# Optimization experiments

Hardware: AMD Instinct MI355X
Metric: run time of the kernel (lower is better)

The kernel has to match this reference:

```python
import jax, jax.numpy as jnp
import numpy as np
import math

DIM = 256; SEQ = 2048; BSZ = 32; NI = 128; NS = 4; ITERS = 3

def _ln(x, g, b):
    m = x.mean(-1, keepdims=True)
    v = ((x - m) ** 2).mean(-1, keepdims=True)
    return (x - m) / jnp.sqrt(v + 1e-5) * g + b

def _norm(x):
    # torch F.normalize: x / ||x||.clamp_min(1e-12)
    return x / jnp.clip(jnp.linalg.norm(x, axis=-1, keepdims=True), 1e-12, None)

def setup_inputs() -> dict:
    key = jax.random.key(0)
    ks = jax.random.split(key, 16)
    def w(k, shape, s=0.02):
        return jax.random.normal(k, shape, jnp.float32) * s
    return {
        'tokens': jax.random.normal(ks[0], (BSZ, SEQ, DIM), jnp.float32),
        'cls_embed': jax.random.normal(ks[1], (BSZ, DIM), jnp.float32),
        'intent_queries': jax.random.normal(ks[2], (NI, DIM), jnp.float32),
        'noise': jax.random.normal(ks[3], (NI, BSZ, NS, DIM), jnp.float32),
        'Wk': w(ks[4], (DIM, DIM)), 'bk': jnp.zeros(DIM, jnp.float32),
        'Wv': w(ks[5], (DIM, DIM)), 'bv': jnp.zeros(DIM, jnp.float32),
        'Wqs': w(ks[6], (DIM, DIM)), 'bqs': jnp.zeros(DIM, jnp.float32),
        'Wqi': w(ks[7], (DIM, DIM)), 'bqi': jnp.zeros(DIM, jnp.float32),
        'ln1_g': jnp.ones(DIM, jnp.float32), 'ln1_b': jnp.zeros(DIM, jnp.float32),
        'ln2_g': jnp.ones(DIM, jnp.float32), 'ln2_b': jnp.zeros(DIM, jnp.float32),
        'Wf1': w(ks[8], (DIM, 2 * DIM)), 'bf1': jnp.zeros(2 * DIM, jnp.float32),
        'Wf2': w(ks[9], (2 * DIM, DIM)), 'bf2': jnp.zeros(DIM, jnp.float32),
        'slot_mu': w(ks[10], (1, NS, DIM)),  # randn*0.02
        'slot_sigma': jnp.ones((1, NS, DIM), jnp.float32) * 0.1,
        'alpha': jnp.float32(1.0),
        'temperature': jnp.float32(1.0),
    }

def reference(tokens, cls_embed, intent_queries, noise, Wk, bk, Wv, bv,
              Wqs, bqs, Wqi, bqi, ln1_g, ln1_b, ln2_g, ln2_b,
              Wf1, bf1, Wf2, bf2, slot_mu, slot_sigma, alpha, temperature):
    scale = 1.0 / math.sqrt(DIM)
    # k/v are identical across the per-intent loop in the original -> compute once
    k = tokens @ Wk + bk  # [B,S,D]
    v = tokens @ Wv + bv  # [B,S,D]
    cls_n = _norm(cls_embed)  # [B,D]

    def per_intent(q, eps):  # q: [D], eps: [B,NS,D]
        qn = _norm(q)
        q_intent = (q @ Wqi + bqi)[None, None, :]  # broadcast over [B,NS,:]
        slots = slot_mu[0] + eps * slot_sigma[0]   # [B,NS,D]
        for _ in range(ITERS):
            q_slot = slots @ Wqs + bqs + q_intent
            logit = jnp.einsum('bnd,bsd->bns', q_slot, k) * scale
            attn = jax.nn.softmax(logit, axis=-1)
            upd = jnp.einsum('bns,bsd->bnd', attn, v)
            slots = _ln(slots + upd, ln1_g, ln1_b)
            h = _ln(slots, ln2_g, ln2_b)
            slots = slots + jax.nn.gelu(h @ Wf1 + bf1, approximate=False) @ Wf2 + bf2
        sn = _norm(slots)                               # [B,NS,D]
        a = jax.nn.softmax(jnp.einsum('bnd,d->bn', sn, qn), axis=-1)
        summ = jnp.einsum('bn,bnd->bd', a, slots)       # slot_summary
        fused = cls_n + alpha * _norm(summ)
        return fused @ qn                               # [B]

    scores = jax.vmap(per_intent)(intent_queries, noise)  # [NI,B]
    logits = scores.T / jnp.maximum(temperature, 1e-4)    # [B,NI]
    return logits
```

## Files before the change

kernel.cpp:

```cpp
#include <hip/hip_runtime.h>
#include <math.h>

#define BSZ 32
#define NI  128

typedef __attribute__((ext_vector_type(8))) _Float16 f16x8;
typedef __attribute__((ext_vector_type(4))) _Float16 f16x4;
typedef __attribute__((ext_vector_type(4))) float    f32x4;

#define MFMA16(a, b, c) __builtin_amdgcn_mfma_f32_16x16x32_f16((a), (b), (c), 0, 0, 0)

#define GLL(g, l) __builtin_amdgcn_global_load_lds(                          \
    (const __attribute__((address_space(1))) void*)(g),                      \
    (__attribute__((address_space(3))) void*)(l), 16, 0, 0)

#define LGKM_BAR() do {                                                      \
    asm volatile("s_waitcnt lgkmcnt(0)" ::: "memory");                       \
    __builtin_amdgcn_sched_barrier(0);                                       \
    __builtin_amdgcn_s_barrier();                                            \
    __builtin_amdgcn_sched_barrier(0); } while (0)

__device__ inline float dot4f(float4 a, float4 b) {
    return a.x * b.x + a.y * b.y + a.z * b.z + a.w * b.w;
}

__device__ inline float4* slp(float* base, int r, int c) {
    return (float4*)(base + r * 256 + ((((c) >> 2) ^ (r & 7)) << 2));
}

__device__ inline void tpose64(const float* __restrict__ src, int Csrc,
                               _Float16* __restrict__ dstT, int KT,
                               int r0, int c0, _Float16 (*tbuf)[72], int tid)
{
#pragma unroll
    for (int it = 0; it < 4; it++) {
        int idx = tid + it * 256;
        int rr = idx >> 4, c4 = idx & 15;
        float4 w = *(const float4*)(src + (size_t)(r0 + rr) * Csrc + c0 + c4 * 4);
        tbuf[c4 * 4 + 0][rr] = (_Float16)w.x;
        tbuf[c4 * 4 + 1][rr] = (_Float16)w.y;
        tbuf[c4 * 4 + 2][rr] = (_Float16)w.z;
        tbuf[c4 * 4 + 3][rr] = (_Float16)w.w;
    }
    __syncthreads();
#pragma unroll
    for (int it = 0; it < 2; it++) {
        int idx = tid + it * 256;
        int orr = idx >> 3, oc8 = idx & 7;
        int n = c0 + orr;
        size_t tile = (size_t)(n >> 4) * KT + (r0 >> 5) + (oc8 >> 2);
        *(f16x8*)(dstT + tile * 512 + (n & 15) * 32 + (oc8 & 3) * 8) = *(const f16x8*)&tbuf[orr][oc8 * 8];
    }
}

__global__ __launch_bounds__(256) void prep(
    const float* __restrict__ Wk, const float* __restrict__ Wv,
    const float* __restrict__ Wqs, const float* __restrict__ Wf1,
    const float* __restrict__ Wf2,
    const float* __restrict__ intent_q, const float* __restrict__ Wqi,
    const float* __restrict__ bqi, const float* __restrict__ bqs,
    const float* __restrict__ cls_embed,
    _Float16* __restrict__ wkT, _Float16* __restrict__ wvT,
    _Float16* __restrict__ wqsT, _Float16* __restrict__ wf1T,
    _Float16* __restrict__ wf2T,
    float* __restrict__ qint2, float* __restrict__ qn, float* __restrict__ clsn)
{
    __shared__ _Float16 tbuf[64][72];
    __shared__ float buf[256];
    __shared__ float red[4];
    const int t = threadIdx.x, blk = blockIdx.x;
    const int lane = t & 63, w = t >> 6;

    if (blk < 112) {
        if (blk < 16)       tpose64(Wk, 256, wkT, 8, (blk >> 2) * 64, (blk & 3) * 64, tbuf, t);
        else if (blk < 32)  { int tt = blk - 16; tpose64(Wv, 256, wvT, 8, (tt >> 2) * 64, (tt & 3) * 64, tbuf, t); }
        else if (blk < 48)  { int tt = blk - 32; tpose64(Wqs, 256, wqsT, 8, (tt >> 2) * 64, (tt & 3) * 64, tbuf, t); }
        else if (blk < 80)  { int tt = blk - 48; tpose64(Wf1, 512, wf1T, 8, (tt & 3) * 64, (tt >> 2) * 64, tbuf, t); }
        else                { int tt = blk - 80; tpose64(Wf2, 256, wf2T, 16, (tt >> 2) * 64, (tt & 3) * 64, tbuf, t); }
    } else if (blk < 240) {
        int i = blk - 112;
        float x = intent_q[(size_t)i * 256 + t];
        buf[t] = x;
        float ss = x * x;
#pragma unroll
        for (int m = 1; m < 64; m <<= 1) ss += __shfl_xor(ss, m, 64);
        if (lane == 0) red[w] = ss;
        __syncthreads();
        float tot = red[0] + red[1] + red[2] + red[3];
        qn[(size_t)i * 256 + t] = x / fmaxf(sqrtf(tot), 1e-12f);
        float acc = bqi[t] + bqs[t];
        for (int e = 0; e < 256; e += 4) {
            const float4 q4 = *(const float4*)&buf[e];
            acc += q4.x * Wqi[(size_t)(e + 0) * 256 + t];
            acc += q4.y * Wqi[(size_t)(e + 1) * 256 + t];
            acc += q4.z * Wqi[(size_t)(e + 2) * 256 + t];
            acc += q4.w * Wqi[(size_t)(e + 3) * 256 + t];
        }
        qint2[(size_t)i * 256 + t] = acc;
    } else {
        int b = blk - 240;
        float x = cls_embed[(size_t)b * 256 + t];
        float ss = x * x;
#pragma unroll
        for (int m = 1; m < 64; m <<= 1) ss += __shfl_xor(ss, m, 64);
        if (lane == 0) red[w] = ss;
        __syncthreads();
        float tot = red[0] + red[1] + red[2] + red[3];
        clsn[(size_t)b * 256 + t] = x / fmaxf(sqrtf(tot), 1e-12f);
    }
}

__global__ __launch_bounds__(512, 2) void kvf_k(
    const float* __restrict__ tokens,
    const _Float16* __restrict__ wkT, const _Float16* __restrict__ wvT,
    const float* __restrict__ bk, const float* __restrict__ bv,
    _Float16* __restrict__ kT, _Float16* __restrict__ vT)
{
    __shared__ __align__(16) _Float16 Sb[2][8192];

    const int t = threadIdx.x, lane = t & 63, w = t >> 6;
    const int l15 = lane & 15, quad = lane >> 4;
    const int lofs = l15 * 32 + quad * 8;
    const int lofsA = ((l15 * 4 + quad) ^ ((l15 >> 1) & 7)) * 8;
    const int bx = blockIdx.x;
    const int b = bx & 31, chunk = bx >> 5;

    f16x8 wk[2][8], wv[2][8];
#pragma unroll
    for (int j = 0; j < 2; j++)
#pragma unroll
        for (int ks = 0; ks < 8; ks++) {
            wk[j][ks] = *(const f16x8*)(wkT + ((size_t)(2 * w + j) * 8 + ks) * 512 + lofs);
            wv[j][ks] = *(const f16x8*)(wvT + ((size_t)(2 * w + j) * 8 + ks) * 512 + lofs);
        }
    f32x4 bi0 = *(const f32x4*)(bk + w * 32 + quad * 4);
    f32x4 bi1 = *(const f32x4*)(bk + w * 32 + 16 + quad * 4);
    const float bv0 = bv[(2 * w) * 16 + l15];
    const float bv1 = bv[(2 * w + 1) * 16 + l15];

    const int rr = t >> 5, d8 = t & 31;
    const float* tbase = tokens + ((size_t)b * 2048 + chunk * 256) * 256 + rr * 256 + d8 * 8;
    const int mskW = ((rr >> 1) & 7) ^ (((d8 >> 2) & 3) << 1);
    const int wofs0 = (d8 >> 2) * 512 + (((rr * 4 + (d8 & 3)) ^ mskW) * 8);
    const int wofs1 = wofs0 + 8 * 512;

    float4 pa0, pa1, pb0, pb1;

#define KVF_LOADS(P) do {                                                    \
        const float* sp_ = tbase + (size_t)(P) * 8192;                       \
        pa0 = *(const float4*)(sp_);                                         \
        pa1 = *(const float4*)(sp_ + 4);                                     \
        pb0 = *(const float4*)(sp_ + 4096);                                  \
        pb1 = *(const float4*)(sp_ + 4100);                                  \
    } while (0)

#define KVF_STAGE(BUF) do {                                                  \
        f16x8 h0, h1;                                                        \
        h0[0] = (_Float16)pa0.x; h0[1] = (_Float16)pa0.y;                    \
        h0[2] = (_Float16)pa0.z; h0[3] = (_Float16)pa0.w;                    \
        h0[4] = (_Float16)pa1.x; h0[5] = (_Float16)pa1.y;                    \
        h0[6] = (_Float16)pa1.z; h0[7] = (_Float16)pa1.w;                    \
        h1[0] = (_Float16)pb0.x; h1[1] = (_Float16)pb0.y;                    \
        h1[2] = (_Float16)pb0.z; h1[3] = (_Float16)pb0.w;                    \
        h1[4] = (_Float16)pb1.x; h1[5] = (_Float16)pb1.y;                    \
        h1[6] = (_Float16)pb1.z; h1[7] = (_Float16)pb1.w;                    \
        *(f16x8*)((BUF) + wofs0) = h0;                                       \
        *(f16x8*)((BUF) + wofs1) = h1;                                       \
    } while (0)

    KVF_LOADS(0);
    KVF_STAGE(&Sb[0][0]);
    LGKM_BAR();

    for (int p = 0; p < 8; p++) {
        if (p < 7) KVF_LOADS(p + 1);
        __builtin_amdgcn_sched_barrier(0);

        const _Float16* lb = &Sb[p & 1][0];
        const int stg0 = chunk * 16 + p * 2;
        const int sp = chunk * 8 + p;

        f16x8 a[2][8];
#pragma unroll
        for (int st = 0; st < 2; st++)
#pragma unroll
            for (int ks = 0; ks < 8; ks++)
                a[st][ks] = *(const f16x8*)(lb + (st * 8 + ks) * 512 + (lofsA ^ ((ks & 3) * 16)));

#pragma unroll
        for (int st = 0; st < 2; st++) {
            f32x4 c0 = {0.f, 0.f, 0.f, 0.f}, c1 = {0.f, 0.f, 0.f, 0.f};
#pragma unroll
            for (int ks = 0; ks < 8; ks++) {
                c0 = MFMA16(wk[0][ks], a[st][ks], c0);
                c1 = MFMA16(wk[1][ks], a[st][ks], c1);
            }
            f16x4 p0, p1;
#pragma unroll
            for (int reg = 0; reg < 4; reg++) {
                p0[reg] = (_Float16)(c0[reg] + bi0[reg]);
                p1[reg] = (_Float16)(c1[reg] + bi1[reg]);
            }
            _Float16* tp = kT + ((size_t)(b * 128 + stg0 + st) * 8 + w) * 512 + l15 * 32;
            *(f16x4*)(tp + (quad >> 1) * 8 + (quad & 1) * 4) = p0;
            *(f16x4*)(tp + (2 + (quad >> 1)) * 8 + (quad & 1) * 4) = p1;
        }

#pragma unroll
        for (int j = 0; j < 2; j++) {
            f32x4 c0 = {0.f, 0.f, 0.f, 0.f}, c1 = {0.f, 0.f, 0.f, 0.f};
#pragma unroll
            for (int ks = 0; ks < 8; ks++) {
                c0 = MFMA16(a[0][ks], wv[j][ks], c0);
                c1 = MFMA16(a[1][ks], wv[j][ks], c1);
            }
            const float bb = j ? bv1 : bv0;
            f16x4 p0, p1;
#pragma unroll
            for (int reg = 0; reg < 4; reg++) {
                p0[reg] = (_Float16)(c0[reg] + bb);
                p1[reg] = (_Float16)(c1[reg] + bb);
            }
            _Float16* tp = vT + ((size_t)(b * 16 + 2 * w + j) * 64 + sp) * 512 + l15 * 32;
            *(f16x4*)(tp + (quad >> 1) * 8 + (quad & 1) * 4) = p0;
            *(f16x4*)(tp + (2 + (quad >> 1)) * 8 + (quad & 1) * 4) = p1;
        }

        if (p < 7) {
            KVF_STAGE(&Sb[(p + 1) & 1][0]);
            LGKM_BAR();
        }
    }
#undef KVF_LOADS
#undef KVF_STAGE
}

__global__ __launch_bounds__(256, 4) void slotq_k(
    const float* __restrict__ noise, const float* __restrict__ slot_mu,
    const float* __restrict__ slot_sigma,
    const _Float16* __restrict__ wqsT, const float* __restrict__ qint2,
    float* __restrict__ slots, _Float16* __restrict__ qsT)
{
    __shared__ float sb[16 * 256];
    const int tid = threadIdx.x, lane = tid & 63, w4 = tid >> 6;
    const int l15 = lane & 15, quad = lane >> 4;
    const int lofs = l15 * 32 + quad * 8;
    const int rt = blockIdx.x;
    const int gr0 = rt * 16;

    {
        const int lr = w4 * 4 + quad;
        const int gr = gr0 + lr;
        const int b = gr >> 9, i = (gr >> 2) & 127, n = gr & 3;
        const float* np = noise + (((size_t)i * BSZ + b) * 4 + n) * 256;
#pragma unroll
        for (int k = 0; k < 4; k++) {
            const int c = k * 64 + l15 * 4;
            float4 mu = *(const float4*)(slot_mu + n * 256 + c);
            float4 sg = *(const float4*)(slot_sigma + n * 256 + c);
            float4 ns = *(const float4*)(np + c);
            float4 o;
            o.x = mu.x + ns.x * sg.x; o.y = mu.y + ns.y * sg.y;
            o.z = mu.z + ns.z * sg.z; o.w = mu.w + ns.w * sg.w;
            *slp(sb, lr, c) = o;
            *(float4*)(slots + (size_t)gr * 256 + c) = o;
        }
    }
    __syncthreads();

    f16x8 bs[8];
#pragma unroll
    for (int ks = 0; ks < 8; ks++) {
        const int c0 = ks * 32 + quad * 8;
        float4 xa = *slp(sb, l15, c0);
        float4 xb = *slp(sb, l15, c0 + 4);
        bs[ks][0] = (_Float16)xa.x; bs[ks][1] = (_Float16)xa.y;
        bs[ks][2] = (_Float16)xa.z; bs[ks][3] = (_Float16)xa.w;
        bs[ks][4] = (_Float16)xb.x; bs[ks][5] = (_Float16)xb.y;
        bs[ks][6] = (_Float16)xb.z; bs[ks][7] = (_Float16)xb.w;
    }
    const int iq = ((gr0 + l15) & 511) >> 2;
#pragma unroll
    for (int d = 0; d < 4; d++) {
        const int dti = w4 * 4 + d;
        f32x4 c = {0.f, 0.f, 0.f, 0.f};
#pragma unroll
        for (int ks = 0; ks < 8; ks++)
            c = MFMA16(*(const f16x8*)(wqsT + ((size_t)dti * 8 + ks) * 512 + lofs), bs[ks], c);
        float4 qi = *(const float4*)(qint2 + (size_t)iq * 256 + dti * 16 + quad * 4);
        f16x4 o;
#pragma unroll
        for (int reg = 0; reg < 4; reg++) o[reg] = (_Float16)((c[reg] + qi[reg]) * 0.0625f);
        *(f16x4*)(qsT + ((size_t)rt * 8 + (dti >> 1)) * 512 + l15 * 32
                  + ((dti & 1) * 2 + (quad >> 1)) * 8 + (quad & 1) * 4) = o;
    }
}

__global__ __launch_bounds__(512, 4) void attn_k(
    const _Float16* __restrict__ qsT, const _Float16* __restrict__ kT,
    const _Float16* __restrict__ vT,
    _Float16* __restrict__ Opart, float* __restrict__ psum4)
{
    __shared__ __align__(16) _Float16 arena[24576];
    __shared__ __align__(16) _Float16 pb[8][640];

    _Float16* KbA = arena;
    _Float16* VbA = arena + 16384;

    const int tid = threadIdx.x, lane = tid & 63, wv = tid >> 6;
    const int l15 = lane & 15, quad = lane >> 4;
    const int lofs = l15 * 32 + quad * 8;
    const int lofsA = ((l15 * 4 + quad) ^ ((l15 >> 1) & 7)) * 8;
    const int lnsw = (lane ^ ((lane >> 3) & 7)) * 8;
    const int bx = blockIdx.x;
    const int b = bx & 31, rb = (bx >> 5) & 3, sk = bx >> 7;
    const int gr0 = b * 512 + rb * 128 + wv * 16;
    const int rt_q = gr0 >> 4;

    _Float16* pw = pb[wv];

    const _Float16* kSrc = kT + ((size_t)(b * 128 + sk * 32) * 8) * 512;
    const _Float16* vSrc = vT + ((size_t)(b * 16) * 64 + sk * 16) * 512;

#pragma unroll
    for (int j = 0; j < 2; j++) {
        const int ee = wv * 2 + j;
        GLL(kSrc + (size_t)((ee >> 3) * 8 + (ee & 7)) * 512 + lnsw,
            KbA + ee * 512 + lane * 8);
    }

    f16x8 q[8];
#pragma unroll
    for (int ks = 0; ks < 8; ks++)
        q[ks] = *(const f16x8*)(qsT + ((size_t)rt_q * 8 + ks) * 512 + lofs);

    f32x4 O[16];
#pragma unroll
    for (int dt = 0; dt < 16; dt++) O[dt] = (f32x4){0.f, 0.f, 0.f, 0.f};
    float ps[4] = {0.f, 0.f, 0.f, 0.f};

    asm volatile("s_waitcnt vmcnt(0)" ::: "memory");
    __builtin_amdgcn_s_barrier();
    __builtin_amdgcn_sched_barrier(0);

    for (int ss = 0; ss < 16; ss++) {
        const int cur = ss & 1;

#pragma unroll
        for (int j = 0; j < 2; j++) {
            const int ee = wv * 2 + j;
            GLL(vSrc + (size_t)(ee * 64 + ss) * 512 + lnsw, VbA + ee * 512 + lane * 8);
        }
        if (ss < 15) {
#pragma unroll
            for (int j = 0; j < 2; j++) {
                const int ee = wv * 2 + j;
                GLL(kSrc + (size_t)((2 * (ss + 1) + (ee >> 3)) * 8 + (ee & 7)) * 512 + lnsw,
                    KbA + (cur ^ 1) * 8192 + ee * 512 + lane * 8);
            }
            asm volatile("s_waitcnt vmcnt(4)" ::: "memory");
        } else {
            asm volatile("s_waitcnt vmcnt(2)" ::: "memory");
        }
        __builtin_amdgcn_s_barrier();
        __builtin_amdgcn_sched_barrier(0);

#pragma unroll
        for (int kt = 0; kt < 2; kt++) {
            const _Float16* kp = KbA + cur * 8192 + (kt * 8) * 512;
            f32x4 c0 = {0.f, 0.f, 0.f, 0.f};
#pragma unroll
            for (int ks = 0; ks < 8; ks++)
                c0 = MFMA16(q[ks], *(const f16x8*)(kp + ks * 512 + lofsA), c0);
            const int col = kt * 16 + l15;
#pragma unroll
            for (int reg = 0; reg < 4; reg++) {
                float p0 = __expf(fminf(c0[reg], 10.5f));
                ps[reg] += p0;
                pw[(quad * 4 + reg) * 40 + col] = (_Float16)p0;
            }
        }

        __builtin_amdgcn_sched_barrier(0);
        asm volatile("s_waitcnt lgkmcnt(0)" ::: "memory");
        if (ss < 15) {
            asm volatile("s_waitcnt vmcnt(2)" ::: "memory");
        } else {
            asm volatile("s_waitcnt vmcnt(0)" ::: "memory");
        }
        __builtin_amdgcn_s_barrier();
        __builtin_amdgcn_sched_barrier(0);

        {
            f16x8 pa = *(const f16x8*)(pw + l15 * 40 + quad * 8);
#pragma unroll
            for (int dt = 0; dt < 16; dt++)
                O[dt] = MFMA16(pa, *(const f16x8*)(VbA + dt * 512 + lofsA), O[dt]);
        }
        __builtin_amdgcn_sched_barrier(0);
        __builtin_amdgcn_s_barrier();
        __builtin_amdgcn_sched_barrier(0);
    }

#pragma unroll
    for (int msk = 1; msk <= 8; msk <<= 1)
#pragma unroll
        for (int reg = 0; reg < 4; reg++) ps[reg] += __shfl_xor(ps[reg], msk, 64);
    if (l15 == 0) {
#pragma unroll
        for (int reg = 0; reg < 4; reg++)
            psum4[(size_t)sk * 16384 + gr0 + quad * 4 + reg] = ps[reg];
    }

    _Float16* ow = arena + wv * 2176;
#pragma unroll
    for (int hd = 0; hd < 2; hd++) {
#pragma unroll
        for (int dt = 0; dt < 8; dt++) {
            const int dti = hd * 8 + dt;
#pragma unroll
            for (int reg = 0; reg < 4; reg++)
                ow[(quad * 4 + reg) * 136 + dt * 16 + l15] = (_Float16)O[dti][reg];
        }
#pragma unroll
        for (int p2 = 0; p2 < 4; p2++) {
            const int u = lane + p2 * 64;
            const int row = u >> 4, col8 = u & 15;
            *(f16x8*)(Opart + ((size_t)sk * 16384 + gr0 + row) * 256 + hd * 128 + col8 * 8) =
                *(const f16x8*)(ow + row * 136 + col8 * 8);
        }
    }
}

__global__ __launch_bounds__(256, 4) void mlp_k(
    const _Float16* __restrict__ Opart, const float* __restrict__ psum4,
    float* __restrict__ slots,
    const float* __restrict__ ln1_g, const float* __restrict__ ln1_b,
    const float* __restrict__ ln2_g, const float* __restrict__ ln2_b,
    const _Float16* __restrict__ wf1T, const float* __restrict__ bf1,
    const _Float16* __restrict__ wf2T, const float* __restrict__ bf2,
    const _Float16* __restrict__ wqsT, const float* __restrict__ qint2,
    _Float16* __restrict__ qsT,
    const float* __restrict__ qn, const float* __restrict__ clsn,
    const float* __restrict__ alphap, const float* __restrict__ tempp,
    float* __restrict__ out, int it)
{
    __shared__ float sl[16 * 256];
    __shared__ float2 st2[16];
    __shared__ __align__(16) _Float16 actL[8192];

    const int tid = threadIdx.x, lane = tid & 63, w4 = tid >> 6;
    const int l15 = lane & 15, quad = lane >> 4;
    const int lofs = l15 * 32 + quad * 8;
    const int lofsA = ((l15 * 4 + quad) ^ ((l15 >> 1) & 7)) * 8;
    const int bx = blockIdx.x;
    const int b = bx & 31, rg = bx >> 5;
    const int R0 = b * 512 + rg * 16;

    {
        const int lr = w4 * 4 + quad;
        const int gr = R0 + lr;
        float l = 0.f;
#pragma unroll
        for (int j = 0; j < 4; j++) l += psum4[(size_t)j * 16384 + gr];
        const float invl = 1.f / l;
        float4 y[4];
        float sm = 0.f, sq = 0.f;
#pragma unroll
        for (int k = 0; k < 4; k++) {
            const int c = k * 64 + l15 * 4;
            float4 o4 = {0.f, 0.f, 0.f, 0.f};
#pragma unroll
            for (int j = 0; j < 4; j++) {
                f16x4 p = *(const f16x4*)(Opart + ((size_t)j * 16384 + gr) * 256 + c);
                o4.x += (float)p[0]; o4.y += (float)p[1];
                o4.z += (float)p[2]; o4.w += (float)p[3];
            }
            float4 s4 = *(const float4*)(slots + (size_t)gr * 256 + c);
            y[k].x = s4.x + o4.x * invl; y[k].y = s4.y + o4.y * invl;
            y[k].z = s4.z + o4.z * invl; y[k].w = s4.w + o4.w * invl;
            sm += y[k].x + y[k].y + y[k].z + y[k].w;
            sq += dot4f(y[k], y[k]);
        }
#pragma unroll
        for (int m = 1; m <= 8; m <<= 1) { sm += __shfl_xor(sm, m, 64); sq += __shfl_xor(sq, m, 64); }
        const float mean = sm * (1.f / 256.f);
        const float rstd = rsqrtf(sq * (1.f / 256.f) - mean * mean + 1e-5f);
        float sm2 = 0.f, sq2 = 0.f;
#pragma unroll
        for (int k = 0; k < 4; k++) {
            const int c = k * 64 + l15 * 4;
            float4 g1 = *(const float4*)(ln1_g + c);
            float4 b1 = *(const float4*)(ln1_b + c);
            float4 x1;
            x1.x = (y[k].x - mean) * rstd * g1.x + b1.x;
            x1.y = (y[k].y - mean) * rstd * g1.y + b1.y;
            x1.z = (y[k].z - mean) * rstd * g1.z + b1.z;
            x1.w = (y[k].w - mean) * rstd * g1.w + b1.w;
            *slp(sl, lr, c) = x1;
            sm2 += x1.x + x1.y + x1.z + x1.w;
            sq2 += dot4f(x1, x1);
        }
#pragma unroll
        for (int m = 1; m <= 8; m <<= 1) { sm2 += __shfl_xor(sm2, m, 64); sq2 += __shfl_xor(sq2, m, 64); }
        const float mean2 = sm2 * (1.f / 256.f);
        const float rstd2 = rsqrtf(sq2 * (1.f / 256.f) - mean2 * mean2 + 1e-5f);
        if (l15 == 0) st2[lr] = make_float2(mean2, rstd2);
    }
    __syncthreads();

    {
        const float2 s2 = st2[l15];
        f16x8 bh[8];
#pragma unroll
        for (int ks = 0; ks < 8; ks++) {
            const int c0 = ks * 32 + quad * 8;
            float4 xa = *slp(sl, l15, c0);
            float4 xb = *slp(sl, l15, c0 + 4);
            float4 ga = *(const float4*)(ln2_g + c0);
            float4 gb = *(const float4*)(ln2_g + c0 + 4);
            float4 ba = *(const float4*)(ln2_b + c0);
            float4 bb2 = *(const float4*)(ln2_b + c0 + 4);
            bh[ks][0] = (_Float16)((xa.x - s2.x) * s2.y * ga.x + ba.x);
            bh[ks][1] = (_Float16)((xa.y - s2.x) * s2.y * ga.y + ba.y);
            bh[ks][2] = (_Float16)((xa.z - s2.x) * s2.y * ga.z + ba.z);
            bh[ks][3] = (_Float16)((xa.w - s2.x) * s2.y * ga.w + ba.w);
            bh[ks][4] = (_Float16)((xb.x - s2.x) * s2.y * gb.x + bb2.x);
            bh[ks][5] = (_Float16)((xb.y - s2.x) * s2.y * gb.y + bb2.y);
            bh[ks][6] = (_Float16)((xb.z - s2.x) * s2.y * gb.z + bb2.z);
            bh[ks][7] = (_Float16)((xb.w - s2.x) * s2.y * gb.w + bb2.w);
        }
#pragma unroll 2
        for (int t8 = 0; t8 < 8; t8++) {
            const int hti = w4 * 8 + t8;
            f32x4 c = {0.f, 0.f, 0.f, 0.f};
#pragma unroll
            for (int ks = 0; ks < 8; ks++)
                c = MFMA16(*(const f16x8*)(wf1T + ((size_t)hti * 8 + ks) * 512 + lofs), bh[ks], c);
            float4 bb = *(const float4*)(bf1 + hti * 16 + quad * 4);
            f16x4 o;
#pragma unroll
            for (int reg = 0; reg < 4; reg++) {
                float xg = c[reg] + bb[reg];
                o[reg] = (_Float16)(0.5f * xg * (1.f + erff(xg * 0.70710678118654752f)));
            }
            const int gA = l15 * 4 + (hti & 1) * 2 + (quad >> 1);
            *(f16x4*)(actL + ((size_t)(hti >> 1)) * 512
                      + ((gA ^ ((l15 >> 1) & 7)) * 8) + (quad & 1) * 4) = o;
        }
    }
    __syncthreads();

    {
        f32x4 c[4];
#pragma unroll
        for (int d = 0; d < 4; d++) {
            const int dti = w4 * 4 + d;
            float4 x4 = *slp(sl, l15, dti * 16 + quad * 4);
            float4 bb = *(const float4*)(bf2 + dti * 16 + quad * 4);
            c[d] = (f32x4){x4.x + bb.x, x4.y + bb.y, x4.z + bb.z, x4.w + bb.w};
        }
        for (int ks = 0; ks < 16; ks++) {
            f16x8 afrag = *(const f16x8*)(actL + (size_t)ks * 512 + lofsA);
#pragma unroll
            for (int d = 0; d < 4; d++)
                c[d] = MFMA16(*(const f16x8*)(wf2T + ((size_t)(w4 * 4 + d) * 16 + ks) * 512 + lofs),
                              afrag, c[d]);
        }
        __syncthreads();
#pragma unroll
        for (int d = 0; d < 4; d++) {
            const int dti = w4 * 4 + d;
            float4 v = {c[d][0], c[d][1], c[d][2], c[d][3]};
            *slp(sl, l15, dti * 16 + quad * 4) = v;
        }
    }
    __syncthreads();

    if (it < 2) {
        f16x8 bs[8];
#pragma unroll
        for (int ks = 0; ks < 8; ks++) {
            const int c0 = ks * 32 + quad * 8;
            float4 xa = *slp(sl, l15, c0);
            float4 xb = *slp(sl, l15, c0 + 4);
            bs[ks][0] = (_Float16)xa.x; bs[ks][1] = (_Float16)xa.y;
            bs[ks][2] = (_Float16)xa.z; bs[ks][3] = (_Float16)xa.w;
            bs[ks][4] = (_Float16)xb.x; bs[ks][5] = (_Float16)xb.y;
            bs[ks][6] = (_Float16)xb.z; bs[ks][7] = (_Float16)xb.w;
        }
        const int iq = rg * 4 + (l15 >> 2);
        const int rtg = b * 32 + rg;
#pragma unroll
        for (int d = 0; d < 4; d++) {
            const int dti = w4 * 4 + d;
            f32x4 c = {0.f, 0.f, 0.f, 0.f};
#pragma unroll
            for (int ks = 0; ks < 8; ks++)
                c = MFMA16(*(const f16x8*)(wqsT + ((size_t)dti * 8 + ks) * 512 + lofs), bs[ks], c);
            float4 qi = *(const float4*)(qint2 + (size_t)iq * 256 + dti * 16 + quad * 4);
            f16x4 o;
#pragma unroll
            for (int reg = 0; reg < 4; reg++) o[reg] = (_Float16)((c[reg] + qi[reg]) * 0.0625f);
            *(f16x4*)(qsT + ((size_t)rtg * 8 + (dti >> 1)) * 512 + l15 * 32
                      + ((dti & 1) * 2 + (quad >> 1)) * 8 + (quad & 1) * 4) = o;
        }
        {
            const int lr2 = tid >> 4, c16 = tid & 15;
#pragma unroll
            for (int q4 = 0; q4 < 4; q4++) {
                float4 v = *slp(sl, lr2, c16 * 16 + q4 * 4);
                *(float4*)(slots + (size_t)(R0 + lr2) * 256 + c16 * 16 + q4 * 4) = v;
            }
        }
    } else {
        const int i = rg * 4 + w4;
        float4 qv = *(const float4*)(qn + (size_t)i * 256 + lane * 4);
        float4 xs[4];
        float st4[4];
#pragma unroll
        for (int n = 0; n < 4; n++) {
            xs[n] = *slp(sl, w4 * 4 + n, lane * 4);
            float ss = dot4f(xs[n], xs[n]);
            float sq = dot4f(xs[n], qv);
#pragma unroll
            for (int m = 1; m < 64; m <<= 1) { ss += __shfl_xor(ss, m, 64); sq += __shfl_xor(sq, m, 64); }
            st4[n] = sq / fmaxf(sqrtf(ss), 1e-12f);
        }
        float mx = fmaxf(fmaxf(st4[0], st4[1]), fmaxf(st4[2], st4[3]));
        float e0 = __expf(st4[0] - mx), e1 = __expf(st4[1] - mx);
        float e2 = __expf(st4[2] - mx), e3 = __expf(st4[3] - mx);
        float inv = 1.f / (e0 + e1 + e2 + e3);
        float4 smv;
        smv.x = (e0 * xs[0].x + e1 * xs[1].x + e2 * xs[2].x + e3 * xs[3].x) * inv;
        smv.y = (e0 * xs[0].y + e1 * xs[1].y + e2 * xs[2].y + e3 * xs[3].y) * inv;
        smv.z = (e0 * xs[0].z + e1 * xs[1].z + e2 * xs[2].z + e3 * xs[3].z) * inv;
        smv.w = (e0 * xs[0].w + e1 * xs[1].w + e2 * xs[2].w + e3 * xs[3].w) * inv;
        float ssm = dot4f(smv, smv);
        float sqn = dot4f(smv, qv);
        float4 cv = *(const float4*)(clsn + (size_t)b * 256 + lane * 4);
        float cq = dot4f(cv, qv);
#pragma unroll
        for (int m = 1; m < 64; m <<= 1) {
            ssm += __shfl_xor(ssm, m, 64);
            sqn += __shfl_xor(sqn, m, 64);
            cq  += __shfl_xor(cq,  m, 64);
        }
        if (lane == 0) {
            float score = cq + alphap[0] * sqn / fmaxf(sqrtf(ssm), 1e-12f);
            out[(size_t)b * NI + i] = score / fmaxf(tempp[0], 1e-4f);
        }
    }
}

extern "C" void kernel_launch(void* const* d_in, const int* in_sizes, int n_in,
                              void* d_out, int out_size, void* d_ws, size_t ws_size,
                              hipStream_t stream)
{
    const float* tokens     = (const float*)d_in[0];
    const float* cls_embed  = (const float*)d_in[1];
    const float* intent_q   = (const float*)d_in[2];
    const float* noise      = (const float*)d_in[3];
    const float* Wk  = (const float*)d_in[4];
    const float* bk  = (const float*)d_in[5];
    const float* Wv  = (const float*)d_in[6];
    const float* bv  = (const float*)d_in[7];
    const float* Wqs = (const float*)d_in[8];
    const float* bqs = (const float*)d_in[9];
    const float* Wqi = (const float*)d_in[10];
    const float* bqi = (const float*)d_in[11];
    const float* ln1g = (const float*)d_in[12];
    const float* ln1b = (const float*)d_in[13];
    const float* ln2g = (const float*)d_in[14];
    const float* ln2b = (const float*)d_in[15];
    const float* Wf1 = (const float*)d_in[16];
    const float* bf1 = (const float*)d_in[17];
    const float* Wf2 = (const float*)d_in[18];
    const float* bf2 = (const float*)d_in[19];
    const float* slot_mu    = (const float*)d_in[20];
    const float* slot_sigma = (const float*)d_in[21];
    const float* alphap = (const float*)d_in[22];
    const float* tempp  = (const float*)d_in[23];
    float* out = (float*)d_out;

    char* base = (char*)d_ws;
    _Float16* qsT   = (_Float16*)(base);
    _Float16* kT    = (_Float16*)(base + 33554432u);
    _Float16* vT    = (_Float16*)(base + 67108864u);
    _Float16* Opart = (_Float16*)(base + 100663296u);
    float* slots    = (float*)(base + 134217728u);
    _Float16* wkT   = (_Float16*)(base + 150994944u);
    _Float16* wvT   = (_Float16*)(base + 151126016u);
    _Float16* wqsT  = (_Float16*)(base + 151257088u);
    _Float16* wf1T  = (_Float16*)(base + 151388160u);
    _Float16* wf2T  = (_Float16*)(base + 151650304u);
    float* qint2    = (float*)(base + 151912448u);
    float* qnb      = (float*)(base + 152043520u);
    float* clsn     = (float*)(base + 152174592u);
    float* psum4    = (float*)(base + 152207360u);

    prep<<<272, 256, 0, stream>>>(Wk, Wv, Wqs, Wf1, Wf2, intent_q, Wqi, bqi, bqs,
                                  cls_embed, wkT, wvT, wqsT, wf1T, wf2T,
                                  qint2, qnb, clsn);
    kvf_k<<<256, 512, 0, stream>>>(tokens, wkT, wvT, bk, bv, kT, vT);
    slotq_k<<<1024, 256, 0, stream>>>(noise, slot_mu, slot_sigma, wqsT, qint2,
                                      slots, qsT);

    for (int it = 0; it < 3; it++) {
        attn_k<<<512, 512, 0, stream>>>(qsT, kT, vT, Opart, psum4);
        mlp_k<<<1024, 256, 0, stream>>>(Opart, psum4, slots,
                                        ln1g, ln1b, ln2g, ln2b,
                                        wf1T, bf1, wf2T, bf2,
                                        wqsT, qint2, qsT,
                                        qnb, clsn, alphap, tempp, out, it);
    }
}
```

Baseline: 489.3 us.

## Process two 16-row query tiles per wave in attention and MLP kernels

The attention kernel now uses 4 waves per block, each handling 32 query rows (two MFMA row tiles) that share each K and V fragment loaded from LDS. The MLP kernel likewise processes 32 rows per block so each weight fragment fetched from global memory feeds two MFMAs, halving the grid. This cuts LDS and global weight traffic per FLOP but doubles accumulator registers (O[2][16]) and LDS use per block, which may reduce occupancy and parallelism.

```diff
diff --git a/kernel.cpp b/kernel.cpp
--- a/kernel.cpp
+++ b/kernel.cpp
@@ -296,13 +296,13 @@
     }
 }
 
-__global__ __launch_bounds__(512, 4) void attn_k(
+__global__ __launch_bounds__(256, 2) void attn_k(
     const _Float16* __restrict__ qsT, const _Float16* __restrict__ kT,
     const _Float16* __restrict__ vT,
     _Float16* __restrict__ Opart, float* __restrict__ psum4)
 {
     __shared__ __align__(16) _Float16 arena[24576];
-    __shared__ __align__(16) _Float16 pb[8][640];
+    __shared__ __align__(16) _Float16 pb[4][1280];
 
     _Float16* KbA = arena;
     _Float16* VbA = arena + 16384;
@@ -314,7 +314,7 @@
     const int lnsw = (lane ^ ((lane >> 3) & 7)) * 8;
     const int bx = blockIdx.x;
     const int b = bx & 31, rb = (bx >> 5) & 3, sk = bx >> 7;
-    const int gr0 = b * 512 + rb * 128 + wv * 16;
+    const int gr0 = b * 512 + rb * 128 + wv * 32;
     const int rt_q = gr0 >> 4;
 
     _Float16* pw = pb[wv];
@@ -323,21 +323,25 @@
     const _Float16* vSrc = vT + ((size_t)(b * 16) * 64 + sk * 16) * 512;
 
 #pragma unroll
-    for (int j = 0; j < 2; j++) {
-        const int ee = wv * 2 + j;
+    for (int j = 0; j < 4; j++) {
+        const int ee = wv * 4 + j;
         GLL(kSrc + (size_t)((ee >> 3) * 8 + (ee & 7)) * 512 + lnsw,
             KbA + ee * 512 + lane * 8);
     }
 
-    f16x8 q[8];
-#pragma unroll
-    for (int ks = 0; ks < 8; ks++)
-        q[ks] = *(const f16x8*)(qsT + ((size_t)rt_q * 8 + ks) * 512 + lofs);
-
-    f32x4 O[16];
-#pragma unroll
-    for (int dt = 0; dt < 16; dt++) O[dt] = (f32x4){0.f, 0.f, 0.f, 0.f};
-    float ps[4] = {0.f, 0.f, 0.f, 0.f};
+    f16x8 q[2][8];
+#pragma unroll
+    for (int m = 0; m < 2; m++)
+#pragma unroll
+        for (int ks = 0; ks < 8; ks++)
+            q[m][ks] = *(const f16x8*)(qsT + ((size_t)(rt_q + m) * 8 + ks) * 512 + lofs);
+
+    f32x4 O[2][16];
+#pragma unroll
+    for (int m = 0; m < 2; m++)
+#pragma unroll
+        for (int dt = 0; dt < 16; dt++) O[m][dt] = (f32x4){0.f, 0.f, 0.f, 0.f};
+    float ps[2][4] = {{0.f, 0.f, 0.f, 0.f}, {0.f, 0.f, 0.f, 0.f}};
 
     asm volatile("s_waitcnt vmcnt(0)" ::: "memory");
     __builtin_amdgcn_s_barrier();
@@ -347,20 +351,20 @@
         const int cur = ss & 1;
 
 #pragma unroll
-        for (int j = 0; j < 2; j++) {
-            const int ee = wv * 2 + j;
+        for (int j = 0; j < 4; j++) {
+            const int ee = wv * 4 + j;
             GLL(vSrc + (size_t)(ee * 64 + ss) * 512 + lnsw, VbA + ee * 512 + lane * 8);
         }
         if (ss < 15) {
 #pragma unroll
-            for (int j = 0; j < 2; j++) {
-                const int ee = wv * 2 + j;
+            for (int j = 0; j < 4; j++) {
+                const int ee = wv * 4 + j;
                 GLL(kSrc + (size_t)((2 * (ss + 1) + (ee >> 3)) * 8 + (ee & 7)) * 512 + lnsw,
                     KbA + (cur ^ 1) * 8192 + ee * 512 + lane * 8);
             }
+            asm volatile("s_waitcnt vmcnt(8)" ::: "memory");
+        } else {
             asm volatile("s_waitcnt vmcnt(4)" ::: "memory");
-        } else {
-            asm volatile("s_waitcnt vmcnt(2)" ::: "memory");
         }
         __builtin_amdgcn_s_barrier();
         __builtin_amdgcn_sched_barrier(0);
@@ -368,23 +372,29 @@
 #pragma unroll
         for (int kt = 0; kt < 2; kt++) {
             const _Float16* kp = KbA + cur * 8192 + (kt * 8) * 512;
-            f32x4 c0 = {0.f, 0.f, 0.f, 0.f};
-#pragma unroll
-            for (int ks = 0; ks < 8; ks++)
-                c0 = MFMA16(q[ks], *(const f16x8*)(kp + ks * 512 + lofsA), c0);
+            f32x4 c0 = {0.f, 0.f, 0.f, 0.f}, c1 = {0.f, 0.f, 0.f, 0.f};
+#pragma unroll
+            for (int ks = 0; ks < 8; ks++) {
+                f16x8 kf = *(const f16x8*)(kp + ks * 512 + lofsA);
+                c0 = MFMA16(q[0][ks], kf, c0);
+                c1 = MFMA16(q[1][ks], kf, c1);
+            }
             const int col = kt * 16 + l15;
 #pragma unroll
             for (int reg = 0; reg < 4; reg++) {
                 float p0 = __expf(fminf(c0[reg], 10.5f));
-                ps[reg] += p0;
+                float p1 = __expf(fminf(c1[reg], 10.5f));
+                ps[0][reg] += p0;
+                ps[1][reg] += p1;
                 pw[(quad * 4 + reg) * 40 + col] = (_Float16)p0;
+                pw[(16 + quad * 4 + reg) * 40 + col] = (_Float16)p1;
             }
         }
 
         __builtin_amdgcn_sched_barrier(0);
         asm volatile("s_waitcnt lgkmcnt(0)" ::: "memory");
         if (ss < 15) {
-            asm volatile("s_waitcnt vmcnt(2)" ::: "memory");
+            asm volatile("s_waitcnt vmcnt(4)" ::: "memory");
         } else {
             asm volatile("s_waitcnt vmcnt(0)" ::: "memory");
         }
@@ -392,10 +402,14 @@
         __builtin_amdgcn_sched_barrier(0);
 
         {
-            f16x8 pa = *(const f16x8*)(pw + l15 * 40 + quad * 8);
-#pragma unroll
-            for (int dt = 0; dt < 16; dt++)
-                O[dt] = MFMA16(pa, *(const f16x8*)(VbA + dt * 512 + lofsA), O[dt]);
+            f16x8 pa0 = *(const f16x8*)(pw + l15 * 40 + quad * 8);
+            f16x8 pa1 = *(const f16x8*)(pw + (16 + l15) * 40 + quad * 8);
+#pragma unroll
+            for (int dt = 0; dt < 16; dt++) {
+                f16x8 vf = *(const f16x8*)(VbA + dt * 512 + lofsA);
+                O[0][dt] = MFMA16(pa0, vf, O[0][dt]);
+                O[1][dt] = MFMA16(pa1, vf, O[1][dt]);
+            }
         }
         __builtin_amdgcn_sched_barrier(0);
         __builtin_amdgcn_s_barrier();
@@ -403,36 +417,42 @@
     }
 
 #pragma unroll
-    for (int msk = 1; msk <= 8; msk <<= 1)
-#pragma unroll
-        for (int reg = 0; reg < 4; reg++) ps[reg] += __shfl_xor(ps[reg], msk, 64);
-    if (l15 == 0) {
-#pragma unroll
-        for (int reg = 0; reg < 4; reg++)
-            psum4[(size_t)sk * 16384 + gr0 + quad * 4 + reg] = ps[reg];
+    for (int m = 0; m < 2; m++) {
+#pragma unroll
+        for (int msk = 1; msk <= 8; msk <<= 1)
+#pragma unroll
+            for (int reg = 0; reg < 4; reg++) ps[m][reg] += __shfl_xor(ps[m][reg], msk, 64);
+        if (l15 == 0) {
+#pragma unroll
+            for (int reg = 0; reg < 4; reg++)
+                psum4[(size_t)sk * 16384 + gr0 + m * 16 + quad * 4 + reg] = ps[m][reg];
+        }
     }
 
     _Float16* ow = arena + wv * 2176;
 #pragma unroll
-    for (int hd = 0; hd < 2; hd++) {
-#pragma unroll
-        for (int dt = 0; dt < 8; dt++) {
-            const int dti = hd * 8 + dt;
-#pragma unroll
-            for (int reg = 0; reg < 4; reg++)
-                ow[(quad * 4 + reg) * 136 + dt * 16 + l15] = (_Float16)O[dti][reg];
-        }
-#pragma unroll
-        for (int p2 = 0; p2 < 4; p2++) {
-            const int u = lane + p2 * 64;
-            const int row = u >> 4, col8 = u & 15;
-            *(f16x8*)(Opart + ((size_t)sk * 16384 + gr0 + row) * 256 + hd * 128 + col8 * 8) =
-                *(const f16x8*)(ow + row * 136 + col8 * 8);
-        }
-    }
-}
-
-__global__ __launch_bounds__(256, 4) void mlp_k(
+    for (int m = 0; m < 2; m++) {
+#pragma unroll
+        for (int hd = 0; hd < 2; hd++) {
+#pragma unroll
+            for (int dt = 0; dt < 8; dt++) {
+                const int dti = hd * 8 + dt;
+#pragma unroll
+                for (int reg = 0; reg < 4; reg++)
+                    ow[(quad * 4 + reg) * 136 + dt * 16 + l15] = (_Float16)O[m][dti][reg];
+            }
+#pragma unroll
+            for (int p2 = 0; p2 < 4; p2++) {
+                const int u = lane + p2 * 64;
+                const int row = u >> 4, col8 = u & 15;
+                *(f16x8*)(Opart + ((size_t)sk * 16384 + gr0 + m * 16 + row) * 256 + hd * 128 + col8 * 8) =
+                    *(const f16x8*)(ow + row * 136 + col8 * 8);
+            }
+        }
+    }
+}
+
+__global__ __launch_bounds__(256, 2) void mlp_k(
     const _Float16* __restrict__ Opart, const float* __restrict__ psum4,
     float* __restrict__ slots,
     const float* __restrict__ ln1_g, const float* __restrict__ ln1_b,
@@ -445,9 +465,9 @@
     const float* __restrict__ alphap, const float* __restrict__ tempp,
     float* __restrict__ out, int it)
 {
-    __shared__ float sl[16 * 256];
-    __shared__ float2 st2[16];
-    __shared__ __align__(16) _Float16 actL[8192];
+    __shared__ float sl[32 * 256];
+    __shared__ float2 st2[32];
+    __shared__ __align__(16) _Float16 actL[16384];
 
     const int tid = threadIdx.x, lane = tid & 63, w4 = tid >> 6;
     const int l15 = lane & 15, quad = lane >> 4;
@@ -455,10 +475,11 @@
     const int lofsA = ((l15 * 4 + quad) ^ ((l15 >> 1) & 7)) * 8;
     const int bx = blockIdx.x;
     const int b = bx & 31, rg = bx >> 5;
-    const int R0 = b * 512 + rg * 16;
-
-    {
-        const int lr = w4 * 4 + quad;
+    const int R0 = b * 512 + rg * 32;
+
+#pragma unroll
+    for (int r2 = 0; r2 < 2; r2++) {
+        const int lr = w4 * 8 + r2 * 4 + quad;
         const int gr = R0 + lr;
         float l = 0.f;
 #pragma unroll
@@ -510,145 +531,176 @@
     __syncthreads();
 
     {
-        const float2 s2 = st2[l15];
-        f16x8 bh[8];
-#pragma unroll
-        for (int ks = 0; ks < 8; ks++) {
-            const int c0 = ks * 32 + quad * 8;
-            float4 xa = *slp(sl, l15, c0);
-            float4 xb = *slp(sl, l15, c0 + 4);
-            float4 ga = *(const float4*)(ln2_g + c0);
-            float4 gb = *(const float4*)(ln2_g + c0 + 4);
-            float4 ba = *(const float4*)(ln2_b + c0);
-            float4 bb2 = *(const float4*)(ln2_b + c0 + 4);
-            bh[ks][0] = (_Float16)((xa.x - s2.x) * s2.y * ga.x + ba.x);
-            bh[ks][1] = (_Float16)((xa.y - s2.x) * s2.y * ga.y + ba.y);
-            bh[ks][2] = (_Float16)((xa.z - s2.x) * s2.y * ga.z + ba.z);
-            bh[ks][3] = (_Float16)((xa.w - s2.x) * s2.y * ga.w + ba.w);
-            bh[ks][4] = (_Float16)((xb.x - s2.x) * s2.y * gb.x + bb2.x);
-            bh[ks][5] = (_Float16)((xb.y - s2.x) * s2.y * gb.y + bb2.y);
-            bh[ks][6] = (_Float16)((xb.z - s2.x) * s2.y * gb.z + bb2.z);
-            bh[ks][7] = (_Float16)((xb.w - s2.x) * s2.y * gb.w + bb2.w);
+        f16x8 bh[2][8];
+#pragma unroll
+        for (int tt = 0; tt < 2; tt++) {
+            const float2 s2 = st2[tt * 16 + l15];
+#pragma unroll
+            for (int ks = 0; ks < 8; ks++) {
+                const int c0 = ks * 32 + quad * 8;
+                float4 xa = *slp(sl, tt * 16 + l15, c0);
+                float4 xb = *slp(sl, tt * 16 + l15, c0 + 4);
+                float4 ga = *(const float4*)(ln2_g + c0);
+                float4 gb = *(const float4*)(ln2_g + c0 + 4);
+                float4 ba = *(const float4*)(ln2_b + c0);
+                float4 bb2 = *(const float4*)(ln2_b + c0 + 4);
+                bh[tt][ks][0] = (_Float16)((xa.x - s2.x) * s2.y * ga.x + ba.x);
+                bh[tt][ks][1] = (_Float16)((xa.y - s2.x) * s2.y * ga.y + ba.y);
+                bh[tt][ks][2] = (_Float16)((xa.z - s2.x) * s2.y * ga.z + ba.z);
+                bh[tt][ks][3] = (_Float16)((xa.w - s2.x) * s2.y * ga.w + ba.w);
+                bh[tt][ks][4] = (_Float16)((xb.x - s2.x) * s2.y * gb.x + bb2.x);
+                bh[tt][ks][5] = (_Float16)((xb.y - s2.x) * s2.y * gb.y + bb2.y);
+                bh[tt][ks][6] = (_Float16)((xb.z - s2.x) * s2.y * gb.z + bb2.z);
+                bh[tt][ks][7] = (_Float16)((xb.w - s2.x) * s2.y * gb.w + bb2.w);
+            }
         }
 #pragma unroll 2
         for (int t8 = 0; t8 < 8; t8++) {
             const int hti = w4 * 8 + t8;
-            f32x4 c = {0.f, 0.f, 0.f, 0.f};
-#pragma unroll
-            for (int ks = 0; ks < 8; ks++)
-                c = MFMA16(*(const f16x8*)(wf1T + ((size_t)hti * 8 + ks) * 512 + lofs), bh[ks], c);
+            f32x4 c0 = {0.f, 0.f, 0.f, 0.f}, c1 = {0.f, 0.f, 0.f, 0.f};
+#pragma unroll
+            for (int ks = 0; ks < 8; ks++) {
+                f16x8 wfrag = *(const f16x8*)(wf1T + ((size_t)hti * 8 + ks) * 512 + lofs);
+                c0 = MFMA16(wfrag, bh[0][ks], c0);
+                c1 = MFMA16(wfrag, bh[1][ks], c1);
+            }
             float4 bb = *(const float4*)(bf1 + hti * 16 + quad * 4);
-            f16x4 o;
+            f16x4 o0, o1;
 #pragma unroll
             for (int reg = 0; reg < 4; reg++) {
-                float xg = c[reg] + bb[reg];
-                o[reg] = (_Float16)(0.5f * xg * (1.f + erff(xg * 0.70710678118654752f)));
+                float xg0 = c0[reg] + bb[reg];
+                float xg1 = c1[reg] + bb[reg];
+                o0[reg] = (_Float16)(0.5f * xg0 * (1.f + erff(xg0 * 0.70710678118654752f)));
+                o1[reg] = (_Float16)(0.5f * xg1 * (1.f + erff(xg1 * 0.70710678118654752f)));
             }
             const int gA = l15 * 4 + (hti & 1) * 2 + (quad >> 1);
-            *(f16x4*)(actL + ((size_t)(hti >> 1)) * 512
-                      + ((gA ^ ((l15 >> 1) & 7)) * 8) + (quad & 1) * 4) = o;
+            const int aofs = ((size_t)(hti >> 1)) * 512 + ((gA ^ ((l15 >> 1) & 7)) * 8) + (quad & 1) * 4;
+            *(f16x4*)(actL + aofs) = o0;
+            *(f16x4*)(actL + 8192 + aofs) = o1;
         }
     }
     __syncthreads();
 
     {
-        f32x4 c[4];
+        f32x4 c[2][4];
+#pragma unroll
+        for (int tt = 0; tt < 2; tt++)
+#pragma unroll
+            for (int d = 0; d < 4; d++) {
+                const int dti = w4 * 4 + d;
+                float4 x4 = *slp(sl, tt * 16 + l15, dti * 16 + quad * 4);
+                float4 bb = *(const float4*)(bf2 + dti * 16 + quad * 4);
+                c[tt][d] = (f32x4){x4.x + bb.x, x4.y + bb.y, x4.z + bb.z, x4.w + bb.w};
+            }
+        for (int ks = 0; ks < 16; ks++) {
+            f16x8 a0 = *(const f16x8*)(actL + (size_t)ks * 512 + lofsA);
+            f16x8 a1 = *(const f16x8*)(actL + 8192 + (size_t)ks * 512 + lofsA);
+#pragma unroll
+            for (int d = 0; d < 4; d++) {
+                f16x8 wfrag = *(const f16x8*)(wf2T + ((size_t)(w4 * 4 + d) * 16 + ks) * 512 + lofs);
+                c[0][d] = MFMA16(wfrag, a0, c[0][d]);
+                c[1][d] = MFMA16(wfrag, a1, c[1][d]);
+            }
+        }
+        __syncthreads();
+#pragma unroll
+        for (int tt = 0; tt < 2; tt++)
+#pragma unroll
+            for (int d = 0; d < 4; d++) {
+                const int dti = w4 * 4 + d;
+                float4 v = {c[tt][d][0], c[tt][d][1], c[tt][d][2], c[tt][d][3]};
+                *slp(sl, tt * 16 + l15, dti * 16 + quad * 4) = v;
+            }
+    }
+    __syncthreads();
+
+    if (it < 2) {
+        f16x8 bs[2][8];
+#pragma unroll
+        for (int tt = 0; tt < 2; tt++)
+#pragma unroll
+            for (int ks = 0; ks < 8; ks++) {
+                const int c0 = ks * 32 + quad * 8;
+                float4 xa = *slp(sl, tt * 16 + l15, c0);
+                float4 xb = *slp(sl, tt * 16 + l15, c0 + 4);
+                bs[tt][ks][0] = (_Float16)xa.x; bs[tt][ks][1] = (_Float16)xa.y;
+                bs[tt][ks][2] = (_Float16)xa.z; bs[tt][ks][3] = (_Float16)xa.w;
+                bs[tt][ks][4] = (_Float16)xb.x; bs[tt][ks][5] = (_Float16)xb.y;
+                bs[tt][ks][6] = (_Float16)xb.z; bs[tt][ks][7] = (_Float16)xb.w;
+            }
+        const int iq0 = rg * 8 + (l15 >> 2);
+        const int rtg0 = b * 32 + rg * 2;
 #pragma unroll
         for (int d = 0; d < 4; d++) {
             const int dti = w4 * 4 + d;
-            float4 x4 = *slp(sl, l15, dti * 16 + quad * 4);
-            float4 bb = *(const float4*)(bf2 + dti * 16 + quad * 4);
-            c[d] = (f32x4){x4.x + bb.x, x4.y + bb.y, x4.z + bb.z, x4.w + bb.w};
-        }
-        for (int ks = 0; ks < 16; ks++) {
-            f16x8 afrag = *(const f16x8*)(actL + (size_t)ks * 512 + lofsA);
-#pragma unroll
-            for (int d = 0; d < 4; d++)
-                c[d] = MFMA16(*(const f16x8*)(wf2T + ((size_t)(w4 * 4 + d) * 16 + ks) * 512 + lofs),
-                              afrag, c[d]);
-        }
-        __syncthreads();
-#pragma unroll
-        for (int d = 0; d < 4; d++) {
-            const int dti = w4 * 4 + d;
-            float4 v = {c[d][0], c[d][1], c[d][2], c[d][3]};
-            *slp(sl, l15, dti * 16 + quad * 4) = v;
-        }
-    }
-    __syncthreads();
-
-    if (it < 2) {
-        f16x8 bs[8];
-#pragma unroll
-        for (int ks = 0; ks < 8; ks++) {
-            const int c0 = ks * 32 + quad * 8;
-            float4 xa = *slp(sl, l15, c0);
-            float4 xb = *slp(sl, l15, c0 + 4);
-            bs[ks][0] = (_Float16)xa.x; bs[ks][1] = (_Float16)xa.y;
-            bs[ks][2] = (_Float16)xa.z; bs[ks][3] = (_Float16)xa.w;
-            bs[ks][4] = (_Float16)xb.x; bs[ks][5] = (_Float16)xb.y;
-            bs[ks][6] = (_Float16)xb.z; bs[ks][7] = (_Float16)xb.w;
-        }
-        const int iq = rg * 4 + (l15 >> 2);
-        const int rtg = b * 32 + rg;
-#pragma unroll
-        for (int d = 0; d < 4; d++) {
-            const int dti = w4 * 4 + d;
-            f32x4 c = {0.f, 0.f, 0.f, 0.f};
-#pragma unroll
-            for (int ks = 0; ks < 8; ks++)
-                c = MFMA16(*(const f16x8*)(wqsT + ((size_t)dti * 8 + ks) * 512 + lofs), bs[ks], c);
-            float4 qi = *(const float4*)(qint2 + (size_t)iq * 256 + dti * 16 + quad * 4);
-            f16x4 o;
-#pragma unroll
-            for (int reg = 0; reg < 4; reg++) o[reg] = (_Float16)((c[reg] + qi[reg]) * 0.0625f);
-            *(f16x4*)(qsT + ((size_t)rtg * 8 + (dti >> 1)) * 512 + l15 * 32
-                      + ((dti & 1) * 2 + (quad >> 1)) * 8 + (quad & 1) * 4) = o;
+            f32x4 c0 = {0.f, 0.f, 0.f, 0.f}, c1 = {0.f, 0.f, 0.f, 0.f};
+#pragma unroll
+            for (int ks = 0; ks < 8; ks++) {
+                f16x8 wfrag = *(const f16x8*)(wqsT + ((size_t)dti * 8 + ks) * 512 + lofs);
+                c0 = MFMA16(wfrag, bs[0][ks], c0);
+                c1 = MFMA16(wfrag, bs[1][ks], c1);
+            }
+            float4 qi0 = *(const float4*)(qint2 + (size_t)iq0 * 256 + dti * 16 + quad * 4);
+            float4 qi1 = *(const float4*)(qint2 + (size_t)(iq0 + 4) * 256 + dti * 16 + quad * 4);
+            f16x4 o0, o1;
+#pragma unroll
+            for (int reg = 0; reg < 4; reg++) {
+                o0[reg] = (_Float16)((c0[reg] + qi0[reg]) * 0.0625f);
+                o1[reg] = (_Float16)((c1[reg] + qi1[reg]) * 0.0625f);
+            }
+            const int qofs = (dti >> 1) * 512 + l15 * 32
+                           + ((dti & 1) * 2 + (quad >> 1)) * 8 + (quad & 1) * 4;
+            *(f16x4*)(qsT + (size_t)rtg0 * 4096 + qofs) = o0;
+            *(f16x4*)(qsT + (size_t)(rtg0 + 1) * 4096 + qofs) = o1;
         }
         {
-            const int lr2 = tid >> 4, c16 = tid & 15;
-#pragma unroll
-            for (int q4 = 0; q4 < 4; q4++) {
-                float4 v = *slp(sl, lr2, c16 * 16 + q4 * 4);
-                *(float4*)(slots + (size_t)(R0 + lr2) * 256 + c16 * 16 + q4 * 4) = v;
+            const int lr2 = tid >> 3, k8 = tid & 7;
+#pragma unroll
+            for (int q4 = 0; q4 < 8; q4++) {
+                float4 v = *slp(sl, lr2, k8 * 32 + q4 * 4);
+                *(float4*)(slots + (size_t)(R0 + lr2) * 256 + k8 * 32 + q4 * 4) = v;
             }
         }
     } else {
-        const int i = rg * 4 + w4;
-        float4 qv = *(const float4*)(qn + (size_t)i * 256 + lane * 4);
-        float4 xs[4];
-        float st4[4];
-#pragma unroll
-        for (int n = 0; n < 4; n++) {
-            xs[n] = *slp(sl, w4 * 4 + n, lane * 4);
-            float ss = dot4f(xs[n], xs[n]);
-            float sq = dot4f(xs[n], qv);
-#pragma unroll
-            for (int m = 1; m < 64; m <<= 1) { ss += __shfl_xor(ss, m, 64); sq += __shfl_xor(sq, m, 64); }
-            st4[n] = sq / fmaxf(sqrtf(ss), 1e-12f);
-        }
-        float mx = fmaxf(fmaxf(st4[0], st4[1]), fmaxf(st4[2], st4[3]));
-        float e0 = __expf(st4[0] - mx), e1 = __expf(st4[1] - mx);
-        float e2 = __expf(st4[2] - mx), e3 = __expf(st4[3] - mx);
-        float inv = 1.f / (e0 + e1 + e2 + e3);
-        float4 smv;
-        smv.x = (e0 * xs[0].x + e1 * xs[1].x + e2 * xs[2].x + e3 * xs[3].x) * inv;
-        smv.y = (e0 * xs[0].y + e1 * xs[1].y + e2 * xs[2].y + e3 * xs[3].y) * inv;
-        smv.z = (e0 * xs[0].z + e1 * xs[1].z + e2 * xs[2].z + e3 * xs[3].z) * inv;
-        smv.w = (e0 * xs[0].w + e1 * xs[1].w + e2 * xs[2].w + e3 * xs[3].w) * inv;
-        float ssm = dot4f(smv, smv);
-        float sqn = dot4f(smv, qv);
-        float4 cv = *(const float4*)(clsn + (size_t)b * 256 + lane * 4);
-        float cq = dot4f(cv, qv);
-#pragma unroll
-        for (int m = 1; m < 64; m <<= 1) {
-            ssm += __shfl_xor(ssm, m, 64);
-            sqn += __shfl_xor(sqn, m, 64);
-            cq  += __shfl_xor(cq,  m, 64);
-        }
-        if (lane == 0) {
-            float score = cq + alphap[0] * sqn / fmaxf(sqrtf(ssm), 1e-12f);
-            out[(size_t)b * NI + i] = score / fmaxf(tempp[0], 1e-4f);
+#pragma unroll
+        for (int ii = 0; ii < 2; ii++) {
+            const int i_loc = w4 * 2 + ii;
+            const int i = rg * 8 + i_loc;
+            float4 qv = *(const float4*)(qn + (size_t)i * 256 + lane * 4);
+            float4 xs[4];
+            float st4[4];
+#pragma unroll
+            for (int n = 0; n < 4; n++) {
+                xs[n] = *slp(sl, i_loc * 4 + n, lane * 4);
+                float ss = dot4f(xs[n], xs[n]);
+                float sq = dot4f(xs[n], qv);
+#pragma unroll
+                for (int m = 1; m < 64; m <<= 1) { ss += __shfl_xor(ss, m, 64); sq += __shfl_xor(sq, m, 64); }
+                st4[n] = sq / fmaxf(sqrtf(ss), 1e-12f);
+            }
+            float mx = fmaxf(fmaxf(st4[0], st4[1]), fmaxf(st4[2], st4[3]));
+            float e0 = __expf(st4[0] - mx), e1 = __expf(st4[1] - mx);
+            float e2 = __expf(st4[2] - mx), e3 = __expf(st4[3] - mx);
+            float inv = 1.f / (e0 + e1 + e2 + e3);
+            float4 smv;
+            smv.x = (e0 * xs[0].x + e1 * xs[1].x + e2 * xs[2].x + e3 * xs[3].x) * inv;
+            smv.y = (e0 * xs[0].y + e1 * xs[1].y + e2 * xs[2].y + e3 * xs[3].y) * inv;
+            smv.z = (e0 * xs[0].z + e1 * xs[1].z + e2 * xs[2].z + e3 * xs[3].z) * inv;
+            smv.w = (e0 * xs[0].w + e1 * xs[1].w + e2 * xs[2].w + e3 * xs[3].w) * inv;
+            float ssm = dot4f(smv, smv);
+            float sqn = dot4f(smv, qv);
+            float4 cv = *(const float4*)(clsn + (size_t)b * 256 + lane * 4);
+            float cq = dot4f(cv, qv);
+#pragma unroll
+            for (int m = 1; m < 64; m <<= 1) {
+                ssm += __shfl_xor(ssm, m, 64);
+                sqn += __shfl_xor(sqn, m, 64);
+                cq  += __shfl_xor(cq,  m, 64);
+            }
+            if (lane == 0) {
+                float score = cq + alphap[0] * sqn / fmaxf(sqrtf(ssm), 1e-12f);
+                out[(size_t)b * NI + i] = score / fmaxf(tempp[0], 1e-4f);
+            }
         }
     }
 }
@@ -707,11 +759,11 @@
                                       slots, qsT);
 
     for (int it = 0; it < 3; it++) {
-        attn_k<<<512, 512, 0, stream>>>(qsT, kT, vT, Opart, psum4);
-        mlp_k<<<1024, 256, 0, stream>>>(Opart, psum4, slots,
-                                        ln1g, ln1b, ln2g, ln2b,
-                                        wf1T, bf1, wf2T, bf2,
-                                        wqsT, qint2, qsT,
-                                        qnb, clsn, alphap, tempp, out, it);
-    }
-}
+        attn_k<<<512, 256, 0, stream>>>(qsT, kT, vT, Opart, psum4);
+        mlp_k<<<512, 256, 0, stream>>>(Opart, psum4, slots,
+                                       ln1g, ln1b, ln2g, ln2b,
+                                       wf1T, bf1, wf2T, bf2,
+                                       wqsT, qint2, qsT,
+                                       qnb, clsn, alphap, tempp, out, it);
+    }
+}
```

New measurement: 438.1 us. 1.12x faster.
